# Performance work log

Hardware: AMD Instinct MI355X
Metric: run time of the kernel (lower is better)

The kernel has to match this reference:

```python
import jax, jax.numpy as jnp
import numpy as np

B, L, C, D = 8, 8192, 256, 256


def setup_inputs() -> dict:
    key = jax.random.key(0)
    ks = jax.random.split(key, 13)
    bound = 1.0 / np.sqrt(C)

    def W(k):
        return jax.random.uniform(k, (C, D), jnp.float32, -bound, bound)

    def b(k):
        return jax.random.uniform(k, (D,), jnp.float32, -bound, bound)

    return {
        "xs": jax.random.normal(ks[0], (B, L, C), jnp.float32),
        # forward-direction params
        "Wh1": W(ks[1]), "bh1": b(ks[2]),
        "Wz1": W(ks[3]), "bz1": b(ks[4]),
        "Ws1": W(ks[5]), "bs1": b(ks[6]),
        "h01": jnp.zeros((1, 1, D), jnp.float32),
        # backward-direction params
        "Wh_1": W(ks[7]), "bh_1": b(ks[8]),
        "Wz_1": W(ks[9]), "bz_1": b(ks[10]),
        "Ws_1": W(ks[11]), "bs_1": b(ks[12]),
        "h0_1": jnp.zeros((1, 1, D), jnp.float32),
    }


def _gru_scan(z, h_tilde, h0):
    """h[t] = z[t]*h_tilde[t] + (1-z[t])*h[t-1], h[-1]=h0. Parallel over time
    via associative scan on the affine maps h -> a*h + b."""
    a = 1.0 - z            # [B, L, D]
    b = z * h_tilde        # [B, L, D]

    def combine(c1, c2):
        a1, b1 = c1
        a2, b2 = c2
        return a1 * a2, a2 * b1 + b2

    A, Bc = jax.lax.associative_scan(combine, (a, b), axis=1)
    return Bc + A * h0     # broadcast h0 [1,1,D]


def reference(xs, Wh1, bh1, Wz1, bz1, Ws1, bs1, h01,
              Wh_1, bh_1, Wz_1, bz_1, Ws_1, bs_1, h0_1):
    sig = jax.nn.sigmoid
    # forward direction
    hf = _gru_scan(sig(xs @ Wz1 + bz1), xs @ Wh1 + bh1, h01) * sig(xs @ Ws1 + bs1)
    # backward direction: reverse time, scan, reverse back
    zr = sig(xs @ Wz_1 + bz_1)
    hr = xs @ Wh_1 + bh_1
    hb = _gru_scan(zr[:, ::-1], hr[:, ::-1], h0_1)[:, ::-1] * sig(xs @ Ws_1 + bs_1)
    return hf + hb
```

## Files before the change

kernel.cpp:

```cpp
#include <hip/hip_runtime.h>
#include <hip/hip_bf16.h>

typedef unsigned short u16;

#define BDIM 8
#define LDIM 8192
#define KDIM 256
#define DDIM 256
#define MTOT 65536
#define NDIM 1536
#define TCH  32
#define NCH  256


typedef float floatx4 __attribute__((ext_vector_type(4)));
typedef short bf16x8 __attribute__((ext_vector_type(8)));

__device__ __forceinline__ u16 f2bf(float f) {
  union { __hip_bfloat16 h; u16 u; } c;
  c.h = __float2bfloat16(f);
  return c.u;
}
__device__ __forceinline__ float bf2f(u16 u) {
  union { unsigned int i; float f; } c;
  c.i = ((unsigned int)u) << 16;
  return c.f;
}
__device__ __forceinline__ float sigmoidf_fast(float x) {
  return __builtin_amdgcn_rcpf(1.0f + __expf(-x));
}
__device__ __forceinline__ void gll16(const u16* g, u16* l) {
  __builtin_amdgcn_global_load_lds((const __attribute__((address_space(1))) void*)g,
                                   (__attribute__((address_space(3))) void*)l, 16, 0, 0);
}

__global__ void prep_weights(const float* __restrict__ Wh1, const float* __restrict__ Wz1,
                             const float* __restrict__ Ws1, const float* __restrict__ Wh_1,
                             const float* __restrict__ Wz_1, const float* __restrict__ Ws_1,
                             const float* __restrict__ bh1, const float* __restrict__ bz1,
                             const float* __restrict__ bs1, const float* __restrict__ bh_1,
                             const float* __restrict__ bz_1, const float* __restrict__ bs_1,
                             u16* __restrict__ WcatT, float* __restrict__ bcat) {
  const int n = blockIdx.x;
  const int k = threadIdx.x;
  const int nn = n & 63;
  const int p = (n & ~63) | ((nn & 15) << 2) | (nn >> 4);
  const int dir = p / 768, r = p % 768;
  int d; const float* W; const float* bb;
  if (r < 512) {
    d = r >> 1;
    if (r & 1) { W = dir ? Wz_1 : Wz1; bb = dir ? bz_1 : bz1; }
    else       { W = dir ? Wh_1 : Wh1; bb = dir ? bh_1 : bh1; }
  } else {
    d = r - 512;
    W = dir ? Ws_1 : Ws1; bb = dir ? bs_1 : bs1;
  }
  WcatT[(size_t)n * KDIM + k] = f2bf(W[k * DDIM + d]);
  if (k == 0) bcat[p] = bb[d];
}

__global__ void convert_xs(const float* __restrict__ xs, u16* __restrict__ Abf) {
  size_t i = ((size_t)blockIdx.x * 256 + threadIdx.x) * 8;
  const float4* s = (const float4*)(xs + i);
  float4 f0 = s[0], f1 = s[1];
  union { u16 u[8]; uint4 v; } t;
  t.u[0] = f2bf(f0.x); t.u[1] = f2bf(f0.y); t.u[2] = f2bf(f0.z); t.u[3] = f2bf(f0.w);
  t.u[4] = f2bf(f1.x); t.u[5] = f2bf(f1.y); t.u[6] = f2bf(f1.z); t.u[7] = f2bf(f1.w);
  *(uint4*)(Abf + i) = t.v;
}

__global__ __launch_bounds__(256) void gemm_kernel(const u16* __restrict__ Abf,
                                                   const u16* __restrict__ WcatT,
                                                   const float* __restrict__ bcat,
                                                   u16* __restrict__ G,
                                                   float* __restrict__ Acc,
                                                   float* __restrict__ Bcc,
                                                   int fuse) {
  __shared__ __align__(16) u16 sm[16384];
  u16* As = sm;
  u16* Bs = sm + 8192;
  const int tid = threadIdx.x;
  const int lane = tid & 63, wave = tid >> 6;
  const int wm = wave >> 1, wn = wave & 1;
  const int q = lane >> 4, r = lane & 15;

  const int xcd = blockIdx.x & 7;
  const int li  = blockIdx.x >> 3;
  const int mt  = xcd * 64 + li / 12;
  const int nt  = li % 12;
  const int m0 = mt * 128, n0 = nt * 128;

  const u16* gA[4]; const u16* gB[4]; u16* lA[4]; u16* lB[4];
#pragma unroll
  for (int j = 0; j < 4; j++) {
    const int bi = wave * 256 + j * 64 + lane;
    const int row = bi >> 3;
    const int kq = (bi & 7) ^ (row & 7);
    gA[j] = Abf   + (size_t)(m0 + row) * KDIM + kq * 8;
    gB[j] = WcatT + (size_t)(n0 + row) * KDIM + kq * 8;
    lA[j] = As + bi * 8;
    lB[j] = Bs + bi * 8;
  }

  floatx4 acc[4][4];
  floatx4 z4 = {0.f, 0.f, 0.f, 0.f};
#pragma unroll
  for (int i = 0; i < 4; i++)
#pragma unroll
    for (int j = 0; j < 4; j++) acc[i][j] = z4;

  for (int k0 = 0; k0 < KDIM; k0 += 64) {
#pragma unroll
    for (int j = 0; j < 4; j++) { gll16(gA[j] + k0, lA[j]); gll16(gB[j] + k0, lB[j]); }
    __syncthreads();
#pragma unroll
    for (int kk = 0; kk < 2; kk++) {
      bf16x8 af[4], bv[4];
#pragma unroll
      for (int i = 0; i < 4; i++) {
        const int row = wm * 64 + i * 16 + r;
        af[i] = *(const bf16x8*)(As + (row * 8 + ((kk * 4 + q) ^ (row & 7))) * 8);
      }
#pragma unroll
      for (int j = 0; j < 4; j++) {
        const int row = wn * 64 + j * 16 + r;
        bv[j] = *(const bf16x8*)(Bs + (row * 8 + ((kk * 4 + q) ^ (row & 7))) * 8);
      }
#pragma unroll
      for (int i = 0; i < 4; i++)
#pragma unroll
        for (int j = 0; j < 4; j++)
          acc[i][j] = __builtin_amdgcn_mfma_f32_16x16x32_bf16(af[i], bv[j], acc[i][j], 0, 0, 0);
    }
    __syncthreads();
  }

  const int pcol = wn * 64 + (r << 2);
  const float4 bv4 = *(const float4*)(bcat + n0 + pcol);
  const int hz = fuse && ((n0 % 768) < 512);
#pragma unroll
  for (int i = 0; i < 4; i++) {
#pragma unroll
    for (int reg = 0; reg < 4; reg++) {
      const int lrow = wm * 64 + i * 16 + q * 4 + reg;
      union { u16 u[4]; uint2 v; } t;
      t.u[0] = f2bf(acc[i][0][reg] + bv4.x);
      t.u[1] = f2bf(acc[i][1][reg] + bv4.y);
      t.u[2] = f2bf(acc[i][2][reg] + bv4.z);
      t.u[3] = f2bf(acc[i][3][reg] + bv4.w);
      *(uint2*)(sm + lrow * 128 + pcol) = t.v;
    }
  }

  __syncthreads();

#pragma unroll
  for (int p = 0; p < 8; p++) {
    const int idx = p * 2048 + tid * 8;
    const int row = idx >> 7, col = idx & 127;
    const uint4 v = *(const uint4*)(sm + idx);
    *(uint4*)(G + (size_t)(m0 + row) * NDIM + n0 + col) = v;
  }

  if (hz) {
    const int cc = wave;
    const int dd = lane;
    const int dirn = n0 / 768;
    const int dbase = (n0 % 768) >> 1;
    const int bb = m0 >> 13;
    const int c0 = (m0 & 8191) >> 5;
    float h = 0.f, P = 1.f;
#pragma unroll 8
    for (int i = 0; i < TCH; ++i) {
      const int tl = dirn ? (TCH - 1 - i) : i;
      const unsigned int hzv = *(const unsigned int*)(sm + (cc * 32 + tl) * 128 + dd * 2);
      const float z = sigmoidf_fast(bf2f((u16)(hzv >> 16)));
      const float a = 1.f - z;
      h = fmaf(a, h, z * bf2f((u16)(hzv & 0xffffu)));
      P *= a;
    }
    const size_t u = (size_t)dirn * 2048 + (size_t)bb * 256 + (size_t)(c0 + cc);
    Acc[u * 256 + dbase + dd] = P;
    Bcc[u * 256 + dbase + dd] = h;
  }
}

__global__ __launch_bounds__(256) void scan_phaseA(const u16* __restrict__ G,
                                                   float* __restrict__ Acc,
                                                   float* __restrict__ Bcc) {
  const int slot = threadIdx.x >> 6, lane = threadIdx.x & 63;
  const int w = blockIdx.x * 4 + slot;
  const int u = w >> 1, half = w & 1;
  const int c = u & 255, b = (u >> 8) & 7, dir = u >> 11;
  const int d0 = half * 128 + lane * 2;
  const u16* p0 = G + (size_t)b * LDIM * NDIM + dir * 768 + d0 * 2;
  float h0 = 0.f, h1 = 0.f, P0 = 1.f, P1 = 1.f;
#pragma unroll 4
  for (int i = 0; i < TCH; ++i) {
    const int t = dir ? (c * TCH + (TCH - 1 - i)) : (c * TCH + i);
    uint2 hz = *(const uint2*)(p0 + (size_t)t * NDIM);
    const u16* q = (const u16*)&hz;
    float z0 = sigmoidf_fast(bf2f(q[1]));
    float z1 = sigmoidf_fast(bf2f(q[3]));
    float a0 = 1.f - z0, a1 = 1.f - z1;
    h0 = fmaf(a0, h0, z0 * bf2f(q[0]));
    h1 = fmaf(a1, h1, z1 * bf2f(q[2]));
    P0 *= a0; P1 *= a1;
  }
  float2 v;
  v.x = P0; v.y = P1;
  *(float2*)(Acc + (size_t)u * 256 + d0) = v;
  v.x = h0; v.y = h1;
  *(float2*)(Bcc + (size_t)u * 256 + d0) = v;
}

__global__ void scan_phaseB(const float* __restrict__ Acc, const float* __restrict__ Bcc,
                            const float* __restrict__ h01, const float* __restrict__ h0_1,
                            float* __restrict__ Pref) {
  const int d = threadIdx.x, b = blockIdx.x, dir = blockIdx.y;
  float h = dir ? h0_1[d] : h01[d];
  const size_t ubase = ((size_t)dir * BDIM + b) * NCH;
  if (dir == 0) {
    for (int c0 = 0; c0 < NCH; c0 += 8) {
      float a[8], bb[8];
#pragma unroll
      for (int j = 0; j < 8; ++j) {
        size_t idx = (ubase + c0 + j) * DDIM + d;
        a[j] = Acc[idx]; bb[j] = Bcc[idx];
      }
#pragma unroll
      for (int j = 0; j < 8; ++j) {
        Pref[(ubase + c0 + j) * DDIM + d] = h;
        h = fmaf(a[j], h, bb[j]);
      }
    }
  } else {
    for (int c0 = NCH - 1; c0 >= 0; c0 -= 8) {
      float a[8], bb[8];
#pragma unroll
      for (int j = 0; j < 8; ++j) {
        size_t idx = (ubase + c0 - j) * DDIM + d;
        a[j] = Acc[idx]; bb[j] = Bcc[idx];
      }
#pragma unroll
      for (int j = 0; j < 8; ++j) {
        Pref[(ubase + c0 - j) * DDIM + d] = h;
        h = fmaf(a[j], h, bb[j]);
      }
    }
  }
}

__global__ __launch_bounds__(512) void scan_phaseC(const u16* __restrict__ G,
                                                   const float* __restrict__ Pref,
                                                   float* __restrict__ out) {
  __shared__ float obuf[TCH * 256];
  const int c = blockIdx.x & 255, b = blockIdx.x >> 8;
  const int wave = threadIdx.x >> 6, lane = threadIdx.x & 63;
  const int dir = wave >> 2;
  const int d0 = (wave & 3) * 64 + lane;
  const int u = dir * 2048 + b * 256 + c;
  float h = Pref[(size_t)u * 256 + d0];
  const u16* ghz = G + (size_t)b * LDIM * NDIM + dir * 768 + d0 * 2;
  const u16* gs  = G + (size_t)b * LDIM * NDIM + dir * 768 + 512 + d0;

  if (dir == 1) {
#pragma unroll
    for (int i = 0; i < TCH; ++i) {
      const int tl = TCH - 1 - i;
      const int t = c * TCH + tl;
      unsigned int hz = *(const unsigned int*)(ghz + (size_t)t * NDIM);
      u16 sv = gs[(size_t)t * NDIM];
      float z = sigmoidf_fast(bf2f((u16)(hz >> 16)));
      h = fmaf(1.f - z, h, z * bf2f((u16)(hz & 0xffff)));
      obuf[tl * 256 + d0] = h * sigmoidf_fast(bf2f(sv));
    }
    __syncthreads();
  } else {
    float ov[TCH];
#pragma unroll
    for (int i = 0; i < TCH; ++i) {
      const int t = c * TCH + i;
      unsigned int hz = *(const unsigned int*)(ghz + (size_t)t * NDIM);
      u16 sv = gs[(size_t)t * NDIM];
      float z = sigmoidf_fast(bf2f((u16)(hz >> 16)));
      h = fmaf(1.f - z, h, z * bf2f((u16)(hz & 0xffff)));
      ov[i] = h * sigmoidf_fast(bf2f(sv));
    }
    __syncthreads();
#pragma unroll
    for (int i = 0; i < TCH; ++i) {
      const int t = c * TCH + i;
      out[((size_t)b * LDIM + t) * DDIM + d0] = ov[i] + obuf[i * 256 + d0];
    }
  }
}

extern "C" void kernel_launch(void* const* d_in, const int* in_sizes, int n_in,
                              void* d_out, int out_size, void* d_ws, size_t ws_size,
                              hipStream_t stream) {
  const float* xs   = (const float*)d_in[0];
  const float* Wh1  = (const float*)d_in[1];
  const float* bh1  = (const float*)d_in[2];
  const float* Wz1  = (const float*)d_in[3];
  const float* bz1  = (const float*)d_in[4];
  const float* Ws1  = (const float*)d_in[5];
  const float* bs1  = (const float*)d_in[6];
  const float* h01  = (const float*)d_in[7];
  const float* Wh_1 = (const float*)d_in[8];
  const float* bh_1 = (const float*)d_in[9];
  const float* Wz_1 = (const float*)d_in[10];
  const float* bz_1 = (const float*)d_in[11];
  const float* Ws_1 = (const float*)d_in[12];
  const float* bs_1 = (const float*)d_in[13];
  const float* h0_1 = (const float*)d_in[14];
  float* out = (float*)d_out;

  char* ws = (char*)d_ws;
  u16* WcatT = (u16*)ws;   ws += (size_t)NDIM * KDIM * 2;
  float* bcat = (float*)ws; ws += (size_t)NDIM * 4;
  u16* Abf = (u16*)ws;     ws += (size_t)MTOT * KDIM * 2;
  u16* G = (u16*)ws;       ws += (size_t)MTOT * NDIM * 2;

  const size_t sumElems = (size_t)2 * BDIM * NCH * DDIM;
  float* Acc; float* Bcc; float* Pref;
  int fuse;
  if ((size_t)(ws - (char*)d_ws) + 3 * sumElems * 4 <= ws_size) {
    Acc  = (float*)ws;
    Bcc  = Acc + sumElems;
    Pref = Bcc + sumElems;
    fuse = 1;
  } else {
    if ((size_t)(ws - (char*)d_ws) > ws_size) return;
    Acc  = (float*)Abf;
    Bcc  = Acc + sumElems;
    Pref = Bcc + sumElems;
    fuse = 0;
  }

  prep_weights<<<dim3(NDIM), dim3(KDIM), 0, stream>>>(
      Wh1, Wz1, Ws1, Wh_1, Wz_1, Ws_1, bh1, bz1, bs1, bh_1, bz_1, bs_1, WcatT, bcat);
  convert_xs<<<dim3(MTOT * KDIM / (256 * 8)), dim3(256), 0, stream>>>(xs, Abf);
  gemm_kernel<<<dim3(6144), dim3(256), 0, stream>>>(Abf, WcatT, bcat, G, Acc, Bcc, fuse);
  if (!fuse)
    scan_phaseA<<<dim3(2048), dim3(256), 0, stream>>>(G, Acc, Bcc);
  scan_phaseB<<<dim3(BDIM, 2), dim3(DDIM), 0, stream>>>(Acc, Bcc, h01, h0_1, Pref);
  scan_phaseC<<<dim3(2048), dim3(512), 0, stream>>>(G, Pref, out);
}
```

Before: 286.3 us.

## Balance bidirectional phaseC work and skip LDS staging for gate output tiles

```diff
diff --git a/kernel.cpp b/kernel.cpp
--- a/kernel.cpp
+++ b/kernel.cpp
@@ -138,31 +138,32 @@
   const int pcol = wn * 64 + (r << 2);
   const float4 bv4 = *(const float4*)(bcat + n0 + pcol);
   const int hz = fuse && ((n0 % 768) < 512);
-#pragma unroll
-  for (int i = 0; i < 4; i++) {
-#pragma unroll
-    for (int reg = 0; reg < 4; reg++) {
-      const int lrow = wm * 64 + i * 16 + q * 4 + reg;
-      union { u16 u[4]; uint2 v; } t;
-      t.u[0] = f2bf(acc[i][0][reg] + bv4.x);
-      t.u[1] = f2bf(acc[i][1][reg] + bv4.y);
-      t.u[2] = f2bf(acc[i][2][reg] + bv4.z);
-      t.u[3] = f2bf(acc[i][3][reg] + bv4.w);
-      *(uint2*)(sm + lrow * 128 + pcol) = t.v;
-    }
-  }
-
-  __syncthreads();
-
-#pragma unroll
-  for (int p = 0; p < 8; p++) {
-    const int idx = p * 2048 + tid * 8;
-    const int row = idx >> 7, col = idx & 127;
-    const uint4 v = *(const uint4*)(sm + idx);
-    *(uint4*)(G + (size_t)(m0 + row) * NDIM + n0 + col) = v;
-  }
 
   if (hz) {
+#pragma unroll
+    for (int i = 0; i < 4; i++) {
+#pragma unroll
+      for (int reg = 0; reg < 4; reg++) {
+        const int lrow = wm * 64 + i * 16 + q * 4 + reg;
+        union { u16 u[4]; uint2 v; } t;
+        t.u[0] = f2bf(acc[i][0][reg] + bv4.x);
+        t.u[1] = f2bf(acc[i][1][reg] + bv4.y);
+        t.u[2] = f2bf(acc[i][2][reg] + bv4.z);
+        t.u[3] = f2bf(acc[i][3][reg] + bv4.w);
+        *(uint2*)(sm + lrow * 128 + pcol) = t.v;
+      }
+    }
+
+    __syncthreads();
+
+#pragma unroll
+    for (int p = 0; p < 8; p++) {
+      const int idx = p * 2048 + tid * 8;
+      const int row = idx >> 7, col = idx & 127;
+      const uint4 v = *(const uint4*)(sm + idx);
+      *(uint4*)(G + (size_t)(m0 + row) * NDIM + n0 + col) = v;
+    }
+
     const int cc = wave;
     const int dd = lane;
     const int dirn = n0 / 768;
@@ -182,6 +183,20 @@
     const size_t u = (size_t)dirn * 2048 + (size_t)bb * 256 + (size_t)(c0 + cc);
     Acc[u * 256 + dbase + dd] = P;
     Bcc[u * 256 + dbase + dd] = h;
+  } else {
+#pragma unroll
+    for (int i = 0; i < 4; i++) {
+#pragma unroll
+      for (int reg = 0; reg < 4; reg++) {
+        const int lrow = wm * 64 + i * 16 + q * 4 + reg;
+        union { u16 u[4]; uint2 v; } t;
+        t.u[0] = f2bf(acc[i][0][reg] + bv4.x);
+        t.u[1] = f2bf(acc[i][1][reg] + bv4.y);
+        t.u[2] = f2bf(acc[i][2][reg] + bv4.z);
+        t.u[3] = f2bf(acc[i][3][reg] + bv4.w);
+        *(uint2*)(G + (size_t)(m0 + lrow) * NDIM + n0 + pcol) = t.v;
+      }
+    }
   }
 }
 
@@ -221,29 +236,29 @@
   float h = dir ? h0_1[d] : h01[d];
   const size_t ubase = ((size_t)dir * BDIM + b) * NCH;
   if (dir == 0) {
-    for (int c0 = 0; c0 < NCH; c0 += 8) {
-      float a[8], bb[8];
-#pragma unroll
-      for (int j = 0; j < 8; ++j) {
+    for (int c0 = 0; c0 < NCH; c0 += 16) {
+      float a[16], bb[16];
+#pragma unroll
+      for (int j = 0; j < 16; ++j) {
         size_t idx = (ubase + c0 + j) * DDIM + d;
         a[j] = Acc[idx]; bb[j] = Bcc[idx];
       }
 #pragma unroll
-      for (int j = 0; j < 8; ++j) {
+      for (int j = 0; j < 16; ++j) {
         Pref[(ubase + c0 + j) * DDIM + d] = h;
         h = fmaf(a[j], h, bb[j]);
       }
     }
   } else {
-    for (int c0 = NCH - 1; c0 >= 0; c0 -= 8) {
-      float a[8], bb[8];
-#pragma unroll
-      for (int j = 0; j < 8; ++j) {
+    for (int c0 = NCH - 1; c0 >= 0; c0 -= 16) {
+      float a[16], bb[16];
+#pragma unroll
+      for (int j = 0; j < 16; ++j) {
         size_t idx = (ubase + c0 - j) * DDIM + d;
         a[j] = Acc[idx]; bb[j] = Bcc[idx];
       }
 #pragma unroll
-      for (int j = 0; j < 8; ++j) {
+      for (int j = 0; j < 16; ++j) {
         Pref[(ubase + c0 - j) * DDIM + d] = h;
         h = fmaf(a[j], h, bb[j]);
       }
@@ -251,48 +266,55 @@
   }
 }
 
-__global__ __launch_bounds__(512) void scan_phaseC(const u16* __restrict__ G,
+__global__ __launch_bounds__(256) void scan_phaseC(const u16* __restrict__ G,
                                                    const float* __restrict__ Pref,
                                                    float* __restrict__ out) {
   __shared__ float obuf[TCH * 256];
   const int c = blockIdx.x & 255, b = blockIdx.x >> 8;
-  const int wave = threadIdx.x >> 6, lane = threadIdx.x & 63;
-  const int dir = wave >> 2;
-  const int d0 = (wave & 3) * 64 + lane;
+  const int dir = threadIdx.x >> 7;
+  const int ld  = threadIdx.x & 127;
+  const int d0 = ld * 2;
   const int u = dir * 2048 + b * 256 + c;
-  float h = Pref[(size_t)u * 256 + d0];
+  const float2 h2 = *(const float2*)(Pref + (size_t)u * 256 + d0);
+  float h0 = h2.x, h1 = h2.y;
   const u16* ghz = G + (size_t)b * LDIM * NDIM + dir * 768 + d0 * 2;
   const u16* gs  = G + (size_t)b * LDIM * NDIM + dir * 768 + 512 + d0;
 
-  if (dir == 1) {
-#pragma unroll
-    for (int i = 0; i < TCH; ++i) {
-      const int tl = TCH - 1 - i;
-      const int t = c * TCH + tl;
-      unsigned int hz = *(const unsigned int*)(ghz + (size_t)t * NDIM);
-      u16 sv = gs[(size_t)t * NDIM];
-      float z = sigmoidf_fast(bf2f((u16)(hz >> 16)));
-      h = fmaf(1.f - z, h, z * bf2f((u16)(hz & 0xffff)));
-      obuf[tl * 256 + d0] = h * sigmoidf_fast(bf2f(sv));
-    }
-    __syncthreads();
-  } else {
-    float ov[TCH];
-#pragma unroll
-    for (int i = 0; i < TCH; ++i) {
-      const int t = c * TCH + i;
-      unsigned int hz = *(const unsigned int*)(ghz + (size_t)t * NDIM);
-      u16 sv = gs[(size_t)t * NDIM];
-      float z = sigmoidf_fast(bf2f((u16)(hz >> 16)));
-      h = fmaf(1.f - z, h, z * bf2f((u16)(hz & 0xffff)));
-      ov[i] = h * sigmoidf_fast(bf2f(sv));
-    }
-    __syncthreads();
-#pragma unroll
-    for (int i = 0; i < TCH; ++i) {
-      const int t = c * TCH + i;
-      out[((size_t)b * LDIM + t) * DDIM + d0] = ov[i] + obuf[i * 256 + d0];
-    }
+#pragma unroll
+  for (int i = 0; i < 16; ++i) {
+    const int tl = dir ? (TCH - 1 - i) : i;
+    const int t = c * TCH + tl;
+    const uint2 hz4 = *(const uint2*)(ghz + (size_t)t * NDIM);
+    const unsigned int s2 = *(const unsigned int*)(gs + (size_t)t * NDIM);
+    const float z0 = sigmoidf_fast(bf2f((u16)(hz4.x >> 16)));
+    const float z1 = sigmoidf_fast(bf2f((u16)(hz4.y >> 16)));
+    h0 = fmaf(1.f - z0, h0, z0 * bf2f((u16)(hz4.x & 0xffffu)));
+    h1 = fmaf(1.f - z1, h1, z1 * bf2f((u16)(hz4.y & 0xffffu)));
+    float2 o;
+    o.x = h0 * sigmoidf_fast(bf2f((u16)(s2 & 0xffffu)));
+    o.y = h1 * sigmoidf_fast(bf2f((u16)(s2 >> 16)));
+    *(float2*)(obuf + tl * 256 + d0) = o;
+  }
+
+  __syncthreads();
+
+#pragma unroll
+  for (int i = 16; i < 32; ++i) {
+    const int tl = dir ? (TCH - 1 - i) : i;
+    const int t = c * TCH + tl;
+    const uint2 hz4 = *(const uint2*)(ghz + (size_t)t * NDIM);
+    const unsigned int s2 = *(const unsigned int*)(gs + (size_t)t * NDIM);
+    const float z0 = sigmoidf_fast(bf2f((u16)(hz4.x >> 16)));
+    const float z1 = sigmoidf_fast(bf2f((u16)(hz4.y >> 16)));
+    h0 = fmaf(1.f - z0, h0, z0 * bf2f((u16)(hz4.x & 0xffffu)));
+    h1 = fmaf(1.f - z1, h1, z1 * bf2f((u16)(hz4.y & 0xffffu)));
+    const float o0 = h0 * sigmoidf_fast(bf2f((u16)(s2 & 0xffffu)));
+    const float o1 = h1 * sigmoidf_fast(bf2f((u16)(s2 >> 16)));
+    const float2 other = *(const float2*)(obuf + tl * 256 + d0);
+    float2 res;
+    res.x = o0 + other.x;
+    res.y = o1 + other.y;
+    *(float2*)(out + ((size_t)b * LDIM + t) * DDIM + d0) = res;
   }
 }
 
@@ -345,5 +367,5 @@
   if (!fuse)
     scan_phaseA<<<dim3(2048), dim3(256), 0, stream>>>(G, Acc, Bcc);
   scan_phaseB<<<dim3(BDIM, 2), dim3(DDIM), 0, stream>>>(Acc, Bcc, h01, h0_1, Pref);
-  scan_phaseC<<<dim3(2048), dim3(512), 0, stream>>>(G, Pref, out);
-}
+  scan_phaseC<<<dim3(2048), dim3(256), 0, stream>>>(G, Pref, out);
+}
```

After: 273.7 us. 4.4% less time.
